# Kernel optimization log

Hardware: AMD Instinct MI355X
Metric: run time of the kernel (lower is better)

The kernel has to match this reference:

```python
import jax, jax.numpy as jnp
import numpy as np

# Model dims (see init_kwargs)
E = 512        # embedding_dim
H = 1536       # hidden_dim
SIZE = 4       # state_space.size (state types per layer)
S = 32         # choices per state type (uniform state size)
L = 12         # num_layers of child network
T = SIZE * L   # total controller steps = 48
V = SIZE * S   # num_embeddings = 128


def setup_inputs() -> dict:
    key = jax.random.key(0)
    ks = jax.random.split(key, 12)
    sc = 0.05
    f32 = jnp.float32
    return {
        "input_id": 0,
        "emb":   (jax.random.normal(ks[0], (V, E)) * sc).astype(f32),
        "W_ih1": (jax.random.normal(ks[1], (4 * H, E)) * sc).astype(f32),
        "W_hh1": (jax.random.normal(ks[2], (4 * H, H)) * sc).astype(f32),
        "b_ih1": (jax.random.normal(ks[3], (4 * H,)) * sc).astype(f32),
        "b_hh1": (jax.random.normal(ks[4], (4 * H,)) * sc).astype(f32),
        "W_ih2": (jax.random.normal(ks[5], (4 * H, H)) * sc).astype(f32),
        "W_hh2": (jax.random.normal(ks[6], (4 * H, H)) * sc).astype(f32),
        "b_ih2": (jax.random.normal(ks[7], (4 * H,)) * sc).astype(f32),
        "b_hh2": (jax.random.normal(ks[8], (4 * H,)) * sc).astype(f32),
        "W_out": (jax.random.normal(ks[9], (T, S, H)) * sc).astype(f32),
        "b_out": (jax.random.normal(ks[10], (T, S)) * sc).astype(f32),
    }


def _lstm_cell(x, h, c, Wih, Whh, bih, bhh):
    # torch.nn.LSTMCell: gates ordered (i, f, g, o)
    g = x @ Wih.T + bih + h @ Whh.T + bhh
    gi, gf, gg, go = jnp.split(g, 4)
    c_new = jax.nn.sigmoid(gf) * c + jax.nn.sigmoid(gi) * jnp.tanh(gg)
    h_new = jax.nn.sigmoid(go) * jnp.tanh(c_new)
    return h_new, c_new


def reference(input_id, emb, W_ih1, W_hh1, b_ih1, b_hh1,
              W_ih2, W_hh2, b_ih2, b_hh2, W_out, b_out):
    x0 = emb[input_id]                      # [E]
    z = jnp.zeros((H,), emb.dtype)

    def step(carry, inp):
        i, Wo, bo = inp                     # Wo: [S,H], bo: [S]
        x, h1, c1, h2, c2 = carry
        h1, c1 = _lstm_cell(x, h1, c1, W_ih1, W_hh1, b_ih1, b_hh1)
        h2, c2 = _lstm_cell(h1, h2, c2, W_ih2, W_hh2, b_ih2, b_hh2)
        logp = jax.nn.log_softmax(Wo @ h2 + bo)   # [S]
        pred = jnp.argmax(logp)
        emb_id = (i % SIZE) * S + pred            # state-space embedding id
        x_next = emb[emb_id]
        return (x_next, h1, c1, h2, c2), logp

    _, scores = jax.lax.scan(step, (x0, z, z, z, z),
                             (jnp.arange(T), W_out, b_out))
    return scores  # [T, S] log-probabilities
```

## Files before the change

kernel.cpp:

```cpp
#include <hip/hip_runtime.h>
#include <math.h>

#define H 1536
#define E 512
#define T 48
#define S 32
#define V 128
#define NB 256
#define BT 512
#define JPB 6
#define ROWS 24
#define RPW 3
#define CHK 24
#define WHH2_B   (64 * 145 * 16)
#define HBUF_B   (64 * 7 * 16)
#define DYN_LDS  (WHH2_B + HBUF_B)

__device__ __forceinline__ float sigf(float x) { return 1.0f / (1.0f + expf(-x)); }
__device__ __forceinline__ float wred(float acc) {
#pragma unroll
    for (int off = 32; off; off >>= 1) acc += __shfl_down(acc, off);
    return acc;
}

#define GLD(p)    __hip_atomic_load((p), __ATOMIC_RELAXED, __HIP_MEMORY_SCOPE_AGENT)
#define GST(p, v) __hip_atomic_store((p), (v), __ATOMIC_RELAXED, __HIP_MEMORY_SCOPE_AGENT)

__device__ __forceinline__ void gbar(unsigned* flags, unsigned& gen) {
    __syncthreads();
    gen++;
    if (threadIdx.x == 0) GST(&flags[blockIdx.x * 16], gen);
    if (threadIdx.x < 64) {
        const int i0 = threadIdx.x * 4;
        for (;;) {
            unsigned a0 = GLD(&flags[(i0 + 0) * 16]);
            unsigned a1 = GLD(&flags[(i0 + 1) * 16]);
            unsigned a2 = GLD(&flags[(i0 + 2) * 16]);
            unsigned a3 = GLD(&flags[(i0 + 3) * 16]);
            bool ok = (a0 >= gen) && (a1 >= gen) && (a2 >= gen) && (a3 >= gen);
            if (__all(ok)) break;
            __builtin_amdgcn_s_sleep(1);
        }
    }
    __syncthreads();
}

__global__ void init_kernel(unsigned* u) {
    for (int i = threadIdx.x; i < 8192; i += 256) u[i] = 0u;
}

__global__ __launch_bounds__(BT, 2) void nas_persist(
    const int* __restrict__ input_id, const float* __restrict__ emb,
    const float* __restrict__ Wih1, const float* __restrict__ Whh1,
    const float* __restrict__ bih1, const float* __restrict__ bhh1,
    const float* __restrict__ Wih2, const float* __restrict__ Whh2,
    const float* __restrict__ bih2, const float* __restrict__ bhh2,
    const float* __restrict__ Wout, const float* __restrict__ bout,
    float* __restrict__ out, float* __restrict__ ws)
{
    const int b = blockIdx.x, tid = threadIdx.x;
    const int wave = tid >> 6, lane = tid & 63;

    unsigned* flags = (unsigned*)ws + 4096;
    float* h2gp[2]  = { ws + 8192, ws + 8192 + H };
    float* candp[2] = { ws + 16384, ws + 16384 + S * H };
    float* xw1g = ws + 114688 + (size_t)b * (V * ROWS);
    float* logitp = ws + 901120;

    extern __shared__ char dyn_lds[];
    float4* whh2s = (float4*)dyn_lds;
    float*  hbuf  = (float*)(dyn_lds + WHH2_B);

    __shared__ float gacc1[ROWS], g2f[ROWS], bsum2[ROWS], zlog[S], h2f[JPB];
    __shared__ float c1s[JPB], c2s[JPB], c1cand[S * JPB];
    __shared__ int   xid_s, pred_s;

    unsigned gen = 0;

    if (tid < JPB) { c2s[tid] = 0.f; GST(h2gp[0] + b * JPB + tid, 0.f); }
    if (tid < ROWS) {
        int r = (tid / JPB) * H + b * JPB + (tid % JPB);
        bsum2[tid] = bih2[r] + bhh2[r];
    }
    if (tid == 0) xid_s = *input_id;

    {
        const int k0 = wave * RPW;
        float4 wiA[RPW], wiB[RPW];
        float  bs[RPW];
#pragma unroll
        for (int i = 0; i < RPW; ++i) {
            int k = k0 + i;
            int r = (k / JPB) * H + b * JPB + (k % JPB);
            const float4* w = (const float4*)(Wih1 + (size_t)r * E);
            wiA[i] = w[lane]; wiB[i] = w[lane + 64];
            bs[i]  = bih1[r] + bhh1[r];
        }
        float4* stage = (float4*)dyn_lds;
        for (int ch = 0; ch < 8; ++ch) {
            const float4* src = (const float4*)(emb + (size_t)ch * 16 * E);
            for (int m = tid; m < 2048; m += BT) stage[m] = src[m];
            __syncthreads();
            for (int vv = 0; vv < 16; ++vv) {
                float4 ea = stage[vv * 128 + lane];
                float4 eb = stage[vv * 128 + 64 + lane];
#pragma unroll
                for (int i = 0; i < RPW; ++i) {
                    float a = wiA[i].x * ea.x + wiA[i].y * ea.y + wiA[i].z * ea.z + wiA[i].w * ea.w
                            + wiB[i].x * eb.x + wiB[i].y * eb.y + wiB[i].z * eb.z + wiB[i].w * eb.w;
                    a = wred(a);
                    if (lane == 0) xw1g[(ch * 16 + vv) * ROWS + (k0 + i)] = a + bs[i];
                }
            }
            __syncthreads();
        }
    }

    for (int k = 0; k < ROWS; ++k) {
        int r = (k / JPB) * H + b * JPB + (k % JPB);
        const float4* src = (const float4*)(Whh2 + (size_t)r * H);
        if (tid < 384) {
            int l = tid / 6, j = tid % 6;
            whh2s[l * 145 + k * 6 + j] = src[tid];
        }
    }
    __syncthreads();

    float w1[RPW][CHK], w2[RPW][CHK];
#pragma unroll
    for (int i = 0; i < RPW; ++i) {
        int k = wave * RPW + i;
        int r = (k / JPB) * H + b * JPB + (k % JPB);
        const float4* p1 = (const float4*)(Whh1 + (size_t)r * H) + lane * 6;
        const float4* p2 = (const float4*)(Wih2 + (size_t)r * H) + lane * 6;
#pragma unroll
        for (int j = 0; j < 6; ++j) {
            float4 v1 = p1[j], v2 = p2[j];
            w1[i][4 * j + 0] = v1.x; w1[i][4 * j + 1] = v1.y;
            w1[i][4 * j + 2] = v1.z; w1[i][4 * j + 3] = v1.w;
            w2[i][4 * j + 0] = v2.x; w2[i][4 * j + 1] = v2.y;
            w2[i][4 * j + 2] = v2.z; w2[i][4 * j + 3] = v2.w;
        }
    }
    __syncthreads();

    if (tid < JPB) {
        const float* xr = xw1g + (size_t)xid_s * ROWS;
        float gi = xr[tid], gg = xr[2 * JPB + tid], go = xr[3 * JPB + tid];
        float cn = sigf(gi) * tanhf(gg);
        c1s[tid] = cn;
        GST(candp[0] + b * JPB + tid, sigf(go) * tanhf(cn));
    }
    gbar(flags, gen);

    const int m0 = (tid / CHK) * 28 + (tid % CHK);
    const int m1 = ((tid + 512) / CHK) * 28 + ((tid + 512) % CHK);
    const int m2 = ((tid + 1024) / CHK) * 28 + ((tid + 1024) % CHK);

    for (int k = 0; k <= T; ++k) {
        float wcol[JPB];
        if (k < T && wave == 0 && lane < S) {
            const float* wp = Wout + ((size_t)k * S + lane) * H + b * JPB;
#pragma unroll
            for (int j = 0; j < JPB; ++j) wcol[j] = wp[j];
        }
        const float* h2src = h2gp[k & 1];
        float u0 = GLD(h2src + tid);
        float u1 = GLD(h2src + tid + 512);
        float u2 = GLD(h2src + tid + 1024);

        if (k > 0) {
            const float* lp = logitp + (size_t)(k & 1) * (S * NB)
                              + (tid >> 4) * NB + (tid & 15) * 16;
            float acc = 0.f;
#pragma unroll
            for (int i = 0; i < 16; ++i) acc += GLD(lp + i);
#pragma unroll
            for (int off = 8; off; off >>= 1) acc += __shfl_down(acc, off, 16);
            if ((tid & 15) == 0)
                zlog[tid >> 4] = acc + bout[(size_t)(k - 1) * S + (tid >> 4)];
        }
        __syncthreads();
        if (k > 0) {
            if (wave == 0) {
                float z = (lane < S) ? zlog[lane] : -1e30f;
                float v = z; int idx = (lane < S) ? lane : 9999;
#pragma unroll
                for (int off = 32; off; off >>= 1) {
                    float ov = __shfl_xor(v, off); int oi = __shfl_xor(idx, off);
                    if (ov > v || (ov == v && oi < idx)) { v = ov; idx = oi; }
                }
                float e = (lane < S) ? expf(z - v) : 0.f;
#pragma unroll
                for (int off = 32; off; off >>= 1) e += __shfl_xor(e, off);
                if (lane == 0) pred_s = idx;
                if (b == 0 && lane < S) out[(size_t)(k - 1) * S + lane] = z - v - logf(e);
            }
            __syncthreads();
        }
        if (k == T) return;
        const int psel = (k > 0) ? pred_s : 0;
        if (k > 0 && tid < JPB) c1s[tid] = c1cand[psel * JPB + tid];

        const float* h1src = candp[k & 1] + (size_t)psel * H;
        float t0 = GLD(h1src + tid);
        float t1 = GLD(h1src + tid + 512);
        float t2 = GLD(h1src + tid + 1024);

        hbuf[m0] = u0; hbuf[m1] = u1; hbuf[m2] = u2;
        __syncthreads();
        float h2c[CHK];
        {
            const float4* hp = (const float4*)hbuf + lane * 7;
#pragma unroll
            for (int j = 0; j < 6; ++j) {
                float4 v = hp[j];
                h2c[4 * j + 0] = v.x; h2c[4 * j + 1] = v.y;
                h2c[4 * j + 2] = v.z; h2c[4 * j + 3] = v.w;
            }
        }
        float ahv[RPW];
#pragma unroll
        for (int i = 0; i < RPW; ++i) {
            int kk = wave * RPW + i;
            const float4* wp = whh2s + lane * 145 + kk * 6;
            float ah = 0.f;
#pragma unroll
            for (int j = 0; j < 6; ++j) {
                float4 v = wp[j];
                ah += v.x * h2c[4 * j + 0] + v.y * h2c[4 * j + 1]
                    + v.z * h2c[4 * j + 2] + v.w * h2c[4 * j + 3];
            }
            ahv[i] = wred(ah);
        }
        __syncthreads();
        hbuf[m0] = t0; hbuf[m1] = t1; hbuf[m2] = t2;
        __syncthreads();
        float h1c[CHK];
        {
            const float4* hp = (const float4*)hbuf + lane * 7;
#pragma unroll
            for (int j = 0; j < 6; ++j) {
                float4 v = hp[j];
                h1c[4 * j + 0] = v.x; h1c[4 * j + 1] = v.y;
                h1c[4 * j + 2] = v.z; h1c[4 * j + 3] = v.w;
            }
        }
        float a1[RPW], a2[RPW];
#pragma unroll
        for (int i = 0; i < RPW; ++i) { a1[i] = 0.f; a2[i] = 0.f; }
#pragma unroll
        for (int kk = 0; kk < CHK; ++kk) {
            float h = h1c[kk];
#pragma unroll
            for (int i = 0; i < RPW; ++i) {
                a1[i] += w1[i][kk] * h;
                a2[i] += w2[i][kk] * h;
            }
        }
#pragma unroll
        for (int i = 0; i < RPW; ++i) {
            int kk = wave * RPW + i;
            float s1 = wred(a1[i]);
            float s2 = wred(a2[i]);
            if (lane == 0) {
                gacc1[kk] = s1;
                g2f[kk]   = s2 + ahv[i] + bsum2[kk];
            }
        }
        __syncthreads();

        if (tid < JPB) {
            float gi = g2f[tid],           gf = g2f[JPB + tid];
            float gg = g2f[2 * JPB + tid], go = g2f[3 * JPB + tid];
            float cn = sigf(gf) * c2s[tid] + sigf(gi) * tanhf(gg);
            c2s[tid] = cn;
            float hn = sigf(go) * tanhf(cn);
            h2f[tid] = hn;
            GST(h2gp[(k + 1) & 1] + b * JPB + tid, hn);
        }
        if (tid < S * JPB) {
            int p = tid / JPB, j = tid % JPB;
            const float* xr = xw1g + (size_t)((k & 3) * S + p) * ROWS;
            float gi = gacc1[j]           + xr[j];
            float gf = gacc1[JPB + j]     + xr[JPB + j];
            float gg = gacc1[2 * JPB + j] + xr[2 * JPB + j];
            float go = gacc1[3 * JPB + j] + xr[3 * JPB + j];
            float cn = sigf(gf) * c1s[j] + sigf(gi) * tanhf(gg);
            c1cand[tid] = cn;
            GST(candp[(k + 1) & 1] + (size_t)p * H + b * JPB + j,
                sigf(go) * tanhf(cn));
        }
        __syncthreads();
        if (wave == 0 && lane < S) {
            float p = 0.f;
#pragma unroll
            for (int j = 0; j < JPB; ++j) p += wcol[j] * h2f[j];
            GST(logitp + (size_t)((k + 1) & 1) * (S * NB) + lane * NB + b, p);
        }
        gbar(flags, gen);
    }
}

extern "C" void kernel_launch(void* const* d_in, const int* in_sizes, int n_in,
                              void* d_out, int out_size, void* d_ws, size_t ws_size,
                              hipStream_t stream) {
    const int*   input_id = (const int*)d_in[0];
    const float* emb  = (const float*)d_in[1];
    const float* Wih1 = (const float*)d_in[2];
    const float* Whh1 = (const float*)d_in[3];
    const float* bih1 = (const float*)d_in[4];
    const float* bhh1 = (const float*)d_in[5];
    const float* Wih2 = (const float*)d_in[6];
    const float* Whh2 = (const float*)d_in[7];
    const float* bih2 = (const float*)d_in[8];
    const float* bhh2 = (const float*)d_in[9];
    const float* Wout = (const float*)d_in[10];
    const float* bout = (const float*)d_in[11];
    float* out = (float*)d_out;
    float* ws  = (float*)d_ws;

    init_kernel<<<1, 256, 0, stream>>>((unsigned*)ws);

    void* args[] = { (void*)&input_id, (void*)&emb,
                     (void*)&Wih1, (void*)&Whh1, (void*)&bih1, (void*)&bhh1,
                     (void*)&Wih2, (void*)&Whh2, (void*)&bih2, (void*)&bhh2,
                     (void*)&Wout, (void*)&bout, (void*)&out, (void*)&ws };
    hipLaunchCooperativeKernel((void*)nas_persist, dim3(NB), dim3(BT), args,
                               DYN_LDS, stream);
}
```

Measured before the change: 1.147 ms.

## Replace per-block flag grid barrier with striped atomic counters and prefetch logits

Each block now does one atomic increment on one of eight striped counters, and eight lanes poll those counters against gen*32. This replaces the scheme where every block wrote its own flag and 64 lanes each polled four flags. The logit partial loads are issued before the h2 and Wout loads so their latency overlaps, and the workspace layout is compacted. The init kernel is replaced by a 512-byte memset and launch bounds are relaxed to one block per CU. The trade-off is atomic contention on the counters in exchange for far fewer polling reads per barrier.

```diff
diff --git a/kernel.cpp b/kernel.cpp
--- a/kernel.cpp
+++ b/kernel.cpp
@@ -16,6 +16,11 @@
 #define HBUF_B   (64 * 7 * 16)
 #define DYN_LDS  (WHH2_B + HBUF_B)
 
+#define LOG_W   4096
+#define H2_W    20480
+#define CAND_W  24576
+#define XW1_W   122880
+
 __device__ __forceinline__ float sigf(float x) { return 1.0f / (1.0f + expf(-x)); }
 __device__ __forceinline__ float wred(float acc) {
 #pragma unroll
@@ -26,30 +31,21 @@
 #define GLD(p)    __hip_atomic_load((p), __ATOMIC_RELAXED, __HIP_MEMORY_SCOPE_AGENT)
 #define GST(p, v) __hip_atomic_store((p), (v), __ATOMIC_RELAXED, __HIP_MEMORY_SCOPE_AGENT)
 
-__device__ __forceinline__ void gbar(unsigned* flags, unsigned& gen) {
+__device__ __forceinline__ void gbar(unsigned* ctr, unsigned& gen) {
     __syncthreads();
     gen++;
-    if (threadIdx.x == 0) GST(&flags[blockIdx.x * 16], gen);
-    if (threadIdx.x < 64) {
-        const int i0 = threadIdx.x * 4;
-        for (;;) {
-            unsigned a0 = GLD(&flags[(i0 + 0) * 16]);
-            unsigned a1 = GLD(&flags[(i0 + 1) * 16]);
-            unsigned a2 = GLD(&flags[(i0 + 2) * 16]);
-            unsigned a3 = GLD(&flags[(i0 + 3) * 16]);
-            bool ok = (a0 >= gen) && (a1 >= gen) && (a2 >= gen) && (a3 >= gen);
-            if (__all(ok)) break;
+    if (threadIdx.x == 0)
+        __hip_atomic_fetch_add(&ctr[(blockIdx.x & 7) * 16], 1u,
+                               __ATOMIC_RELAXED, __HIP_MEMORY_SCOPE_AGENT);
+    if (threadIdx.x < 8) {
+        const unsigned tgt = gen * 32u;
+        while (GLD(&ctr[threadIdx.x * 16]) < tgt)
             __builtin_amdgcn_s_sleep(1);
-        }
     }
     __syncthreads();
 }
 
-__global__ void init_kernel(unsigned* u) {
-    for (int i = threadIdx.x; i < 8192; i += 256) u[i] = 0u;
-}
-
-__global__ __launch_bounds__(BT, 2) void nas_persist(
+__global__ __launch_bounds__(BT, 1) void nas_persist(
     const int* __restrict__ input_id, const float* __restrict__ emb,
     const float* __restrict__ Wih1, const float* __restrict__ Whh1,
     const float* __restrict__ bih1, const float* __restrict__ bhh1,
@@ -61,11 +57,11 @@
     const int b = blockIdx.x, tid = threadIdx.x;
     const int wave = tid >> 6, lane = tid & 63;
 
-    unsigned* flags = (unsigned*)ws + 4096;
-    float* h2gp[2]  = { ws + 8192, ws + 8192 + H };
-    float* candp[2] = { ws + 16384, ws + 16384 + S * H };
-    float* xw1g = ws + 114688 + (size_t)b * (V * ROWS);
-    float* logitp = ws + 901120;
+    unsigned* ctr = (unsigned*)ws;
+    float* logitp = ws + LOG_W;
+    float* h2gp[2]  = { ws + H2_W,   ws + H2_W + H };
+    float* candp[2] = { ws + CAND_W, ws + CAND_W + S * H };
+    float* xw1g = ws + XW1_W + (size_t)b * (V * ROWS);
 
     extern __shared__ char dyn_lds[];
     float4* whh2s = (float4*)dyn_lds;
@@ -151,30 +147,35 @@
         c1s[tid] = cn;
         GST(candp[0] + b * JPB + tid, sigf(go) * tanhf(cn));
     }
-    gbar(flags, gen);
+    gbar(ctr, gen);
 
     const int m0 = (tid / CHK) * 28 + (tid % CHK);
     const int m1 = ((tid + 512) / CHK) * 28 + ((tid + 512) % CHK);
     const int m2 = ((tid + 1024) / CHK) * 28 + ((tid + 1024) % CHK);
 
     for (int k = 0; k <= T; ++k) {
-        float wcol[JPB];
-        if (k < T && wave == 0 && lane < S) {
-            const float* wp = Wout + ((size_t)k * S + lane) * H + b * JPB;
-#pragma unroll
-            for (int j = 0; j < JPB; ++j) wcol[j] = wp[j];
+        float pv[16];
+        const float* lp = logitp + (size_t)(k & 1) * (S * NB)
+                          + (tid >> 4) * NB + (tid & 15) * 16;
+        if (k > 0) {
+#pragma unroll
+            for (int i = 0; i < 16; ++i) pv[i] = GLD(lp + i);
         }
         const float* h2src = h2gp[k & 1];
         float u0 = GLD(h2src + tid);
         float u1 = GLD(h2src + tid + 512);
         float u2 = GLD(h2src + tid + 1024);
+        float wcol[JPB];
+        if (k < T && wave == 0 && lane < S) {
+            const float* wp = Wout + ((size_t)k * S + lane) * H + b * JPB;
+#pragma unroll
+            for (int j = 0; j < JPB; ++j) wcol[j] = wp[j];
+        }
 
         if (k > 0) {
-            const float* lp = logitp + (size_t)(k & 1) * (S * NB)
-                              + (tid >> 4) * NB + (tid & 15) * 16;
             float acc = 0.f;
 #pragma unroll
-            for (int i = 0; i < 16; ++i) acc += GLD(lp + i);
+            for (int i = 0; i < 16; ++i) acc += pv[i];
 #pragma unroll
             for (int off = 8; off; off >>= 1) acc += __shfl_down(acc, off, 16);
             if ((tid & 15) == 0)
@@ -298,7 +299,7 @@
             for (int j = 0; j < JPB; ++j) p += wcol[j] * h2f[j];
             GST(logitp + (size_t)((k + 1) & 1) * (S * NB) + lane * NB + b, p);
         }
-        gbar(flags, gen);
+        gbar(ctr, gen);
     }
 }
 
@@ -320,7 +321,7 @@
     float* out = (float*)d_out;
     float* ws  = (float*)d_ws;
 
-    init_kernel<<<1, 256, 0, stream>>>((unsigned*)ws);
+    hipMemsetAsync(d_ws, 0, 512, stream);
 
     void* args[] = { (void*)&input_id, (void*)&emb,
                      (void*)&Wih1, (void*)&Whh1, (void*)&bih1, (void*)&bhh1,
```

Result: slower. 1.207 ms (+5.2%).
